# Kernel tuning notes

Measured on AMD Instinct MI355X. Metric: run time of the kernel, lower is better.

The kernel has to match this reference:

```python
import jax, jax.numpy as jnp
import numpy as np

B, C, D, H = 2, 1024, 1024, 16
DH = D // H
EPS = 1e-8


def setup_inputs() -> dict:
    key = jax.random.key(0)
    ks = jax.random.split(key, 12)
    s = 0.02
    return {
        "x": jax.random.normal(ks[0], (B, C, D), dtype=jnp.float32),
        "rms_w": jnp.ones((C, D), dtype=jnp.float32),
        "rms_b": jnp.zeros((C, D), dtype=jnp.float32),
        "Wqkv": jax.random.normal(ks[1], (3 * D, D), dtype=jnp.float32) * s,
        "Wout": jax.random.normal(ks[2], (D, D), dtype=jnp.float32) * s,
        "bout": jnp.zeros((D,), dtype=jnp.float32),
        "Wf": jax.random.normal(ks[3], (D, D), dtype=jnp.float32) * s,
        "bf": jnp.zeros((D,), dtype=jnp.float32),
        "Ww": jax.random.normal(ks[4], (D, D), dtype=jnp.float32) * s,
        "bw": jnp.zeros((D,), dtype=jnp.float32),
        "Wv": jax.random.normal(ks[5], (D, D), dtype=jnp.float32) * s,
        "bv": jnp.zeros((D,), dtype=jnp.float32),
        "beta": jnp.ones((1,), dtype=jnp.float32),
    }


def _rope_cos_sin(C, dh):
    # faithful to source: theta = 10000 ** (-2*(i-1)/dh), i in [0, dh//2)
    i = jnp.arange(dh // 2, dtype=jnp.float32)
    theta = 10000.0 ** (-2.0 * (i - 1.0) / dh)            # [dh//2]
    ang = jnp.arange(C, dtype=jnp.float32)[:, None] * theta  # [C, dh//2]
    return jnp.cos(ang), jnp.sin(ang)


def _rotate(t, cos, sin):
    # equivalent to einsum('bhci,cij->bhcj', t, R) with the source R
    ev, od = t[..., 0::2], t[..., 1::2]          # [B,H,C,dh//2]
    out_ev = ev * cos + od * sin
    out_od = -ev * sin + od * cos
    return jnp.stack([out_ev, out_od], axis=-1).reshape(t.shape)


def _rmsnorm(x, w, b):
    rms = jnp.sqrt(jnp.mean(x * x, axis=-1, keepdims=True) + EPS)
    return w * (x / rms) + b


def _attention(x, Wqkv, Wout, bout):
    qkv = x @ Wqkv.T                               # [B,C,3D]
    q, k, v = jnp.split(qkv, 3, axis=-1)
    def heads(t):
        return t.reshape(B, C, H, DH).transpose(0, 2, 1, 3)  # [B,H,C,dh]
    q, k, v = heads(q), heads(k), heads(v)
    cos, sin = _rope_cos_sin(C, DH)
    qr = _rotate(q, cos, sin)
    kr = _rotate(k, cos, sin)
    scale = 1.0 / jnp.sqrt(jnp.float32(DH))
    num = jnp.exp(jnp.einsum('bhid,bhjd->bhij', qr, kr) * scale)
    den = jnp.sum(jnp.exp(jnp.einsum('bhid,bhjd->bhij', q, k) * scale),
                  axis=-1, keepdims=True)
    attn = num / den
    mask = jnp.tril(jnp.ones((C, C), dtype=bool))
    attn = jnp.where(mask[None, None], attn, 0.0)
    y = attn @ v                                   # [B,H,C,dh]
    y = y.transpose(0, 2, 1, 3).reshape(B, C, D)
    return y @ Wout.T + bout


def _ffn(x, Wf, bf, Ww, bw, Wv, bv, beta):
    h = x @ Wf.T + bf
    wx = h @ Ww.T + bw
    swish = wx * jax.nn.sigmoid(beta * wx)
    return swish * (h @ Wv.T + bv)


def reference(x, rms_w, rms_b, Wqkv, Wout, bout, Wf, bf, Ww, bw, Wv, bv, beta):
    # dropout p is identity in eval mode
    x = _rmsnorm(x, rms_w, rms_b)
    x = x + _attention(x, Wqkv, Wout, bout)
    x = _rmsnorm(x, rms_w, rms_b)   # same shared RMSNorm module applied twice
    x = x + _ffn(x, Wf, bf, Ww, bw, Wv, bv, beta)
    return x
```

## Files before the change

### kernel.cpp

```cpp
#include <hip/hip_runtime.h>
#include <math.h>

#define B_ 2
#define C_ 1024
#define D_ 1024
#define H_ 16
#define DH_ 64
#define EPSF 1e-8f
#define BK 32

typedef __bf16 bf16;
typedef __attribute__((ext_vector_type(4))) __bf16 bf16x4;
typedef __attribute__((ext_vector_type(8))) __bf16 bf16x8;
typedef __attribute__((ext_vector_type(4))) float f32x4;

__device__ inline f32x4 mfma16(bf16x8 a, bf16x8 b, f32x4 c) {
  return __builtin_amdgcn_mfma_f32_16x16x32_bf16(a, b, c, 0, 0, 0);
}

__device__ inline void async16(const bf16* g, bf16* l) {
  __builtin_amdgcn_global_load_lds((const __attribute__((address_space(1))) void*)g,
                                   (__attribute__((address_space(3))) void*)l, 16, 0, 0);
}

__device__ inline float rope_theta(float i) {
  return exp2f(-13.287712379549449f * (2.0f * (i - 1.0f) * (1.0f / 64.0f)));
}

__global__ __launch_bounds__(256) void cvt_rms_kernel(const float* __restrict__ wqkv,
                                                      const float* __restrict__ wout,
                                                      const float* __restrict__ wf,
                                                      const float* __restrict__ www,
                                                      const float* __restrict__ wv,
                                                      bf16* __restrict__ wdst,
                                                      const float* __restrict__ x,
                                                      const float* __restrict__ rw,
                                                      const float* __restrict__ rb,
                                                      bf16* __restrict__ xout) {
  __shared__ float red[4];
  int t = threadIdx.x;
  if (blockIdx.x < 7 * 1024) {
    int seg = blockIdx.x >> 10;
    int local = (blockIdx.x & 1023) * 1024 + t * 4;
    const float* src = seg < 3 ? wqkv + (size_t)seg * (D_ * D_)
                     : seg == 3 ? wout : seg == 4 ? wf : seg == 5 ? www : wv;
    float4 v = *(const float4*)(src + local);
    bf16x4 o;
    o[0] = (bf16)v.x; o[1] = (bf16)v.y; o[2] = (bf16)v.z; o[3] = (bf16)v.w;
    *(bf16x4*)(wdst + (size_t)seg * (D_ * D_) + local) = o;
    return;
  }
  int row = blockIdx.x - 7 * 1024;
  int c = row & (C_ - 1);
  float4 xv = *(const float4*)(x + (size_t)row * D_ + t * 4);
  float ss = xv.x * xv.x + xv.y * xv.y + xv.z * xv.z + xv.w * xv.w;
#pragma unroll
  for (int m = 1; m < 64; m <<= 1) ss += __shfl_xor(ss, m, 64);
  if ((t & 63) == 0) red[t >> 6] = ss;
  __syncthreads();
  float tot = red[0] + red[1] + red[2] + red[3];
  float inv = rsqrtf(tot * (1.0f / D_) + EPSF);
  float4 wv4 = *(const float4*)(rw + (size_t)c * D_ + t * 4);
  float4 bv4 = *(const float4*)(rb + (size_t)c * D_ + t * 4);
  bf16x4 ov;
  ov[0] = (bf16)(wv4.x * (xv.x * inv) + bv4.x);
  ov[1] = (bf16)(wv4.y * (xv.y * inv) + bv4.y);
  ov[2] = (bf16)(wv4.z * (xv.z * inv) + bv4.z);
  ov[3] = (bf16)(wv4.w * (xv.w * inv) + bv4.w);
  *(bf16x4*)(xout + (size_t)row * D_ + t * 4) = ov;
}

__global__ __launch_bounds__(256) void rmsnorm_bf16_kernel(const bf16* __restrict__ x,
                                                           const float* __restrict__ w,
                                                           const float* __restrict__ b,
                                                           bf16* __restrict__ out) {
  int row = blockIdx.x;
  int c = row & (C_ - 1);
  int t = threadIdx.x;
  bf16x4 xv = *(const bf16x4*)(x + (size_t)row * D_ + t * 4);
  float f0 = (float)xv[0], f1 = (float)xv[1], f2 = (float)xv[2], f3 = (float)xv[3];
  float ss = f0 * f0 + f1 * f1 + f2 * f2 + f3 * f3;
#pragma unroll
  for (int m = 1; m < 64; m <<= 1) ss += __shfl_xor(ss, m, 64);
  __shared__ float red[4];
  if ((t & 63) == 0) red[t >> 6] = ss;
  __syncthreads();
  float tot = red[0] + red[1] + red[2] + red[3];
  float inv = rsqrtf(tot * (1.0f / D_) + EPSF);
  float4 wv = *(const float4*)(w + (size_t)c * D_ + t * 4);
  float4 bv = *(const float4*)(b + (size_t)c * D_ + t * 4);
  bf16x4 ov;
  ov[0] = (bf16)(wv.x * (f0 * inv) + bv.x);
  ov[1] = (bf16)(wv.y * (f1 * inv) + bv.y);
  ov[2] = (bf16)(wv.z * (f2 * inv) + bv.z);
  ov[3] = (bf16)(wv.w * (f3 * inv) + bv.w);
  *(bf16x4*)(out + (size_t)row * D_ + t * 4) = ov;
}

template <int BMt, int BNt>
__global__ __launch_bounds__(256) void gemm_lds(const bf16* __restrict__ A,
                                                const bf16* __restrict__ W,
                                                const float* __restrict__ bias,
                                                const bf16* __restrict__ R,
                                                bf16* __restrict__ Cout,
                                                int M, int N, int K) {
  constexpr int MT = BMt / 32;
  constexpr int NT = BNt / 32;
  __shared__ bf16 sa[BMt * BK];
  __shared__ bf16 sb[BNt * BK];
  int t = threadIdx.x, l = t & 63, w = t >> 6;
  int m0 = blockIdx.y * BMt;
  int n0 = blockIdx.x * BNt;
  int wm = (w >> 1) * (BMt / 2), wn = (w & 1) * (BNt / 2);
  int lm = l & 15, lq = l >> 4;
  f32x4 acc[MT][NT] = {};

  for (int k0 = 0; k0 < K; k0 += BK) {
    __syncthreads();
    if constexpr (BMt >= 64) {
#pragma unroll
      for (int p = 0; p < BMt / 64; ++p) {
        int lin = p * 256 + t;
        async16(A + (size_t)(m0 + (lin >> 2)) * K + k0 + (lin & 3) * 8, sa + lin * 8);
      }
    } else {
      if (t < BMt * 4)
        async16(A + (size_t)(m0 + (t >> 2)) * K + k0 + (t & 3) * 8, sa + t * 8);
    }
#pragma unroll
    for (int p = 0; p < BNt / 64; ++p) {
      int lin = p * 256 + t;
      async16(W + (size_t)(n0 + (lin >> 2)) * K + k0 + (lin & 3) * 8, sb + lin * 8);
    }
    __syncthreads();
    bf16x8 af[MT], bfr[NT];
#pragma unroll
    for (int mt = 0; mt < MT; ++mt)
      af[mt] = *(const bf16x8*)(sa + (wm + mt * 16 + lm) * BK + lq * 8);
#pragma unroll
    for (int nt = 0; nt < NT; ++nt)
      bfr[nt] = *(const bf16x8*)(sb + (wn + nt * 16 + lm) * BK + lq * 8);
#pragma unroll
    for (int mt = 0; mt < MT; ++mt)
#pragma unroll
      for (int nt = 0; nt < NT; ++nt)
        acc[mt][nt] = mfma16(af[mt], bfr[nt], acc[mt][nt]);
  }
#pragma unroll
  for (int mt = 0; mt < MT; ++mt)
#pragma unroll
    for (int nt = 0; nt < NT; ++nt) {
      int col = n0 + wn + nt * 16 + lm;
      float bb = bias ? bias[col] : 0.0f;
#pragma unroll
      for (int r = 0; r < 4; ++r) {
        int row = m0 + wm + mt * 16 + lq * 4 + r;
        float v = acc[mt][nt][r] + bb;
        if (R) v += (float)R[(size_t)row * N + col];
        Cout[(size_t)row * N + col] = (bf16)v;
      }
    }
}

__global__ __launch_bounds__(256) void gemm_qkv_kernel(const bf16* __restrict__ A,
                                                       const bf16* __restrict__ W,
                                                       bf16* __restrict__ qkv,
                                                       bf16* __restrict__ vt) {
  constexpr int BMt = 128, BNt = 64, MT = 4, NT = 2;
  const int N = 3 * D_, K = D_;
  __shared__ bf16 sa[BMt * BK];
  __shared__ bf16 sb[BNt * BK];
  __shared__ bf16 tv[64 * 136];
  int t = threadIdx.x, l = t & 63, w = t >> 6;
  int m0 = blockIdx.y * BMt;
  int n0 = blockIdx.x * BNt;
  int wm = (w >> 1) * 64, wn = (w & 1) * 32;
  int lm = l & 15, lq = l >> 4;
  f32x4 acc[MT][NT] = {};

  for (int k0 = 0; k0 < K; k0 += BK) {
    __syncthreads();
#pragma unroll
    for (int p = 0; p < 2; ++p) {
      int lin = p * 256 + t;
      async16(A + (size_t)(m0 + (lin >> 2)) * K + k0 + (lin & 3) * 8, sa + lin * 8);
    }
    async16(W + (size_t)(n0 + (t >> 2)) * K + k0 + (t & 3) * 8, sb + t * 8);
    __syncthreads();
    bf16x8 af[MT], bfr[NT];
#pragma unroll
    for (int mt = 0; mt < MT; ++mt)
      af[mt] = *(const bf16x8*)(sa + (wm + mt * 16 + lm) * BK + lq * 8);
#pragma unroll
    for (int nt = 0; nt < NT; ++nt)
      bfr[nt] = *(const bf16x8*)(sb + (wn + nt * 16 + lm) * BK + lq * 8);
#pragma unroll
    for (int mt = 0; mt < MT; ++mt)
#pragma unroll
      for (int nt = 0; nt < NT; ++nt)
        acc[mt][nt] = mfma16(af[mt], bfr[nt], acc[mt][nt]);
  }
  if (n0 < 2 * D_) {
#pragma unroll
    for (int mt = 0; mt < MT; ++mt)
#pragma unroll
      for (int nt = 0; nt < NT; ++nt) {
        int col = n0 + wn + nt * 16 + lm;
#pragma unroll
        for (int r = 0; r < 4; ++r) {
          int row = m0 + wm + mt * 16 + lq * 4 + r;
          qkv[(size_t)row * N + col] = (bf16)acc[mt][nt][r];
        }
      }
  } else {
#pragma unroll
    for (int mt = 0; mt < MT; ++mt)
#pragma unroll
      for (int nt = 0; nt < NT; ++nt) {
        int dh = wn + nt * 16 + lm;
#pragma unroll
        for (int r = 0; r < 4; ++r)
          tv[dh * 136 + wm + mt * 16 + lq * 4 + r] = (bf16)acc[mt][nt][r];
      }
    __syncthreads();
    int h = (n0 - 2 * D_) >> 6;
    int bb = m0 >> 10;
    int mloc = m0 & 1023;
    size_t vbase = (size_t)((bb * H_ + h) * DH_) * C_;
#pragma unroll
    for (int p = 0; p < 4; ++p) {
      int lin = p * 256 + t;
      int dh = lin >> 4;
      int mm = (lin & 15) * 8;
      *(int4*)(vt + vbase + (size_t)dh * C_ + mloc + mm) = *(int4*)(tv + dh * 136 + mm);
    }
  }
}

__global__ __launch_bounds__(256) void gemm_ffn_kernel(const bf16* __restrict__ A,
                                                       const bf16* __restrict__ Ww,
                                                       const bf16* __restrict__ Wv,
                                                       const float* __restrict__ bw,
                                                       const float* __restrict__ bv,
                                                       const bf16* __restrict__ x3,
                                                       const float* __restrict__ beta_p,
                                                       float* __restrict__ out) {
  __shared__ bf16 sa[64 * BK];
  __shared__ bf16 sb1[64 * BK];
  __shared__ bf16 sb2[64 * BK];
  int t = threadIdx.x, l = t & 63, w = t >> 6;
  int m0 = blockIdx.y * 64, n0 = blockIdx.x * 64;
  int wm = (w >> 1) * 32, wn = (w & 1) * 32;
  int lm = l & 15, lq = l >> 4;
  float beta = beta_p[0];
  f32x4 acc1[2][2] = {}, acc2[2][2] = {};

  for (int k0 = 0; k0 < D_; k0 += BK) {
    __syncthreads();
    async16(A + (size_t)(m0 + (t >> 2)) * D_ + k0 + (t & 3) * 8, sa + t * 8);
    async16(Ww + (size_t)(n0 + (t >> 2)) * D_ + k0 + (t & 3) * 8, sb1 + t * 8);
    async16(Wv + (size_t)(n0 + (t >> 2)) * D_ + k0 + (t & 3) * 8, sb2 + t * 8);
    __syncthreads();
    bf16x8 af[2], b1f[2], b2f[2];
#pragma unroll
    for (int mt = 0; mt < 2; ++mt)
      af[mt] = *(const bf16x8*)(sa + (wm + mt * 16 + lm) * BK + lq * 8);
#pragma unroll
    for (int nt = 0; nt < 2; ++nt) {
      b1f[nt] = *(const bf16x8*)(sb1 + (wn + nt * 16 + lm) * BK + lq * 8);
      b2f[nt] = *(const bf16x8*)(sb2 + (wn + nt * 16 + lm) * BK + lq * 8);
    }
#pragma unroll
    for (int mt = 0; mt < 2; ++mt)
#pragma unroll
      for (int nt = 0; nt < 2; ++nt) {
        acc1[mt][nt] = mfma16(af[mt], b1f[nt], acc1[mt][nt]);
        acc2[mt][nt] = mfma16(af[mt], b2f[nt], acc2[mt][nt]);
      }
  }
#pragma unroll
  for (int mt = 0; mt < 2; ++mt)
#pragma unroll
    for (int nt = 0; nt < 2; ++nt) {
      int col = n0 + wn + nt * 16 + lm;
      float bbw = bw[col], bbv = bv[col];
#pragma unroll
      for (int r = 0; r < 4; ++r) {
        int row = m0 + wm + mt * 16 + lq * 4 + r;
        float z = acc1[mt][nt][r] + bbw;
        float g = acc2[mt][nt][r] + bbv;
        float sw = z / (1.0f + __expf(-beta * z));
        out[(size_t)row * D_ + col] = (float)x3[(size_t)row * D_ + col] + sw * g;
      }
    }
}

__global__ __launch_bounds__(256) void attn_kernel(const bf16* __restrict__ qkv,
                                                   const bf16* __restrict__ vt,
                                                   float* __restrict__ yp,
                                                   float* __restrict__ dp) {
  __shared__ bf16 sk[64 * 72];
  __shared__ bf16 skr[64 * 72];
  __shared__ bf16 sv[64 * 72];
  __shared__ bf16 pl[4][16 * 72];
  int t = threadIdx.x, l = t & 63, w = t >> 6;
  int blk = blockIdx.x;
  int it = blk >> 6;
  int r6 = blk & 63;
  int b = r6 >> 5;
  int h = (r6 >> 1) & 15;
  int half = r6 & 1;
  int i_base = it * 64 + w * 16;
  int lm = l & 15, lq = l >> 4;
  const float scale = 0.125f;
  int jf = half << 9;

  size_t hq = (size_t)h * DH_;
  size_t qrow = (size_t)(b * C_ + i_base + lm) * (3 * D_) + hq;
  bf16x8 qp[2], qrf[2];
  float cq = (float)(i_base + lm);
#pragma unroll
  for (int kk = 0; kk < 2; ++kk) {
    qp[kk] = *(const bf16x8*)(qkv + qrow + kk * 32 + lq * 8);
#pragma unroll
    for (int j = 0; j < 4; ++j) {
      float ip = (float)(kk * 16 + lq * 4 + j);
      float ang = cq * rope_theta(ip);
      float sv_, cv_;
      __sincosf(ang, &sv_, &cv_);
      float qe = (float)qp[kk][2 * j], qo = (float)qp[kk][2 * j + 1];
      qrf[kk][2 * j] = (bf16)(qe * cv_ + qo * sv_);
      qrf[kk][2 * j + 1] = (bf16)(qo * cv_ - qe * sv_);
    }
  }

  float den[4] = {0.f, 0.f, 0.f, 0.f};
  f32x4 yacc[4] = {};
  int i_max = i_base + 15;
  size_t kbase = (size_t)(b * C_) * (3 * D_) + D_ + hq;
  size_t vtbase = (size_t)((b * H_ + h) * DH_) * C_;
  int sr = t >> 3;
  int sc = (t & 7) * 8;
  float th0 = rope_theta((float)((sc >> 1) + 0));
  float th1 = rope_theta((float)((sc >> 1) + 1));
  float th2 = rope_theta((float)((sc >> 1) + 2));
  float th3 = rope_theta((float)((sc >> 1) + 3));

  float cA0, sA0, cA1, sA1, cA2, sA2, cA3, sA3;
  float cB0, sB0, cB1, sB1, cB2, sB2, cB3, sB3;
  float C0, S0, C1, S1, C2, S2, C3, S3;
#define INITP(P)                       \
  {                                    \
    float a;                           \
    a = (float)(jf + sr) * th##P;      \
    __sincosf(a, &sA##P, &cA##P);      \
    a = (float)(jf + 32 + sr) * th##P; \
    __sincosf(a, &sB##P, &cB##P);      \
    a = 64.0f * th##P;                 \
    __sincosf(a, &S##P, &C##P);        \
  }
  INITP(0) INITP(1) INITP(2) INITP(3)
#undef INITP

  int4 pk0, pk1, pv0, pv1;
#define FETCH_TILE(J0)                                                          \
  pk0 = *(const int4*)(qkv + kbase + (size_t)((J0) + sr) * (3 * D_) + sc);      \
  pk1 = *(const int4*)(qkv + kbase + (size_t)((J0) + 32 + sr) * (3 * D_) + sc); \
  pv0 = *(const int4*)(vt + vtbase + (size_t)sr * C_ + (J0) + sc);              \
  pv1 = *(const int4*)(vt + vtbase + (size_t)(32 + sr) * C_ + (J0) + sc);

  FETCH_TILE(jf)

  for (int j0 = jf; j0 < jf + 512; j0 += 64) {
    __syncthreads();
    *(int4*)(sk + sr * 72 + sc) = pk0;
    *(int4*)(sk + (32 + sr) * 72 + sc) = pk1;
    *(int4*)(sv + sr * 72 + sc) = pv0;
    *(int4*)(sv + (32 + sr) * 72 + sc) = pv1;
    {
      bf16x8 k0 = *(bf16x8*)&pk0, k1 = *(bf16x8*)&pk1;
      bf16x8 r0, r1;
#define ROT2(KV, RV, CC, SS, J)                           \
  {                                                       \
    float e = (float)KV[2 * J], o = (float)KV[2 * J + 1]; \
    RV[2 * J] = (bf16)(e * CC + o * SS);                  \
    RV[2 * J + 1] = (bf16)(o * CC - e * SS);              \
  }
      ROT2(k0, r0, cA0, sA0, 0) ROT2(k0, r0, cA1, sA1, 1)
      ROT2(k0, r0, cA2, sA2, 2) ROT2(k0, r0, cA3, sA3, 3)
      ROT2(k1, r1, cB0, sB0, 0) ROT2(k1, r1, cB1, sB1, 1)
      ROT2(k1, r1, cB2, sB2, 2) ROT2(k1, r1, cB3, sB3, 3)
#undef ROT2
#define STEP(CX, SX, P)               \
  {                                   \
    float nc = CX * C##P - SX * S##P; \
    SX = SX * C##P + CX * S##P;       \
    CX = nc;                          \
  }
      STEP(cA0, sA0, 0) STEP(cA1, sA1, 1) STEP(cA2, sA2, 2) STEP(cA3, sA3, 3)
      STEP(cB0, sB0, 0) STEP(cB1, sB1, 1) STEP(cB2, sB2, 2) STEP(cB3, sB3, 3)
#undef STEP
      *(int4*)(skr + sr * 72 + sc) = *(int4*)&r0;
      *(int4*)(skr + (32 + sr) * 72 + sc) = *(int4*)&r1;
    }
    __syncthreads();
    if (j0 + 64 < jf + 512) {
      FETCH_TILE(j0 + 64)
    }
#pragma unroll
    for (int js = 0; js < 64; js += 16) {
      bf16x8 kf0 = *(const bf16x8*)(sk + (js + lm) * 72 + lq * 8);
      bf16x8 kf1 = *(const bf16x8*)(sk + (js + lm) * 72 + 32 + lq * 8);
      f32x4 s = {0.f, 0.f, 0.f, 0.f};
      s = mfma16(qp[0], kf0, s);
      s = mfma16(qp[1], kf1, s);
#pragma unroll
      for (int r = 0; r < 4; ++r) den[r] += __expf(s[r] * scale);
    }
    if (j0 <= i_max) {
#pragma unroll
      for (int js = 0; js < 64; js += 16) {
        bf16x8 kf0 = *(const bf16x8*)(skr + (js + lm) * 72 + lq * 8);
        bf16x8 kf1 = *(const bf16x8*)(skr + (js + lm) * 72 + 32 + lq * 8);
        f32x4 s = {0.f, 0.f, 0.f, 0.f};
        s = mfma16(qrf[0], kf0, s);
        s = mfma16(qrf[1], kf1, s);
#pragma unroll
        for (int r = 0; r < 4; ++r) {
          int jg = j0 + js + lm;
          int ig = i_base + lq * 4 + r;
          float p = (jg <= ig) ? __expf(s[r] * scale) : 0.0f;
          pl[w][(lq * 4 + r) * 72 + js + lm] = (bf16)p;
        }
      }
      __builtin_amdgcn_wave_barrier();
      bf16x8 pf0 = *(const bf16x8*)(pl[w] + lm * 72 + lq * 8);
      bf16x8 pf1 = *(const bf16x8*)(pl[w] + lm * 72 + 32 + lq * 8);
#pragma unroll
      for (int tt = 0; tt < 4; ++tt) {
        bf16x8 vf0 = *(const bf16x8*)(sv + (tt * 16 + lm) * 72 + lq * 8);
        bf16x8 vf1 = *(const bf16x8*)(sv + (tt * 16 + lm) * 72 + 32 + lq * 8);
        yacc[tt] = mfma16(pf0, vf0, mfma16(pf1, vf1, yacc[tt]));
      }
      __builtin_amdgcn_wave_barrier();
    }
  }
#undef FETCH_TILE
#pragma unroll
  for (int r = 0; r < 4; ++r) {
    float d = den[r];
    d += __shfl_xor(d, 1, 64);
    d += __shfl_xor(d, 2, 64);
    d += __shfl_xor(d, 4, 64);
    d += __shfl_xor(d, 8, 64);
    if (lm == 0) dp[(size_t)blk * 64 + w * 16 + lq * 4 + r] = d;
  }
  size_t yb = (size_t)blk * 4096;
#pragma unroll
  for (int tt = 0; tt < 4; ++tt)
#pragma unroll
    for (int r = 0; r < 4; ++r)
      yp[yb + (size_t)(w * 16 + lq * 4 + r) * 64 + tt * 16 + lm] = yacc[tt][r];
}

__global__ __launch_bounds__(256) void combine_kernel(const float* __restrict__ yp,
                                                      const float* __restrict__ dp,
                                                      bf16* __restrict__ y) {
  int cb = blockIdx.x;
  int it = cb >> 5;
  int b = (cb >> 4) & 1;
  int h = cb & 15;
  int t = threadIdx.x;
  int row = t >> 2;
  int cg = (t & 3) * 16;
  size_t p0 = (size_t)(cb * 2) * 4096 + (size_t)row * 64 + cg;
  size_t p1 = p0 + 4096;
  float inv = 1.0f / (dp[(size_t)(cb * 2) * 64 + row] + dp[(size_t)(cb * 2 + 1) * 64 + row]);
  bf16x8 o0, o1;
#pragma unroll
  for (int c = 0; c < 8; ++c) o0[c] = (bf16)((yp[p0 + c] + yp[p1 + c]) * inv);
#pragma unroll
  for (int c = 0; c < 8; ++c) o1[c] = (bf16)((yp[p0 + 8 + c] + yp[p1 + 8 + c]) * inv);
  size_t ob = (size_t)(b * C_ + it * 64 + row) * D_ + h * DH_ + cg;
  *(bf16x8*)(y + ob) = o0;
  *(bf16x8*)(y + ob + 8) = o1;
}

extern "C" void kernel_launch(void* const* d_in, const int* in_sizes, int n_in,
                              void* d_out, int out_size, void* d_ws, size_t ws_size,
                              hipStream_t stream) {
  const float* x = (const float*)d_in[0];
  const float* rms_w = (const float*)d_in[1];
  const float* rms_b = (const float*)d_in[2];
  const float* Wqkv = (const float*)d_in[3];
  const float* Wout = (const float*)d_in[4];
  const float* bout = (const float*)d_in[5];
  const float* Wf = (const float*)d_in[6];
  const float* bfp = (const float*)d_in[7];
  const float* Ww = (const float*)d_in[8];
  const float* bw = (const float*)d_in[9];
  const float* Wv = (const float*)d_in[10];
  const float* bv = (const float*)d_in[11];
  const float* beta = (const float*)d_in[12];
  float* out = (float*)d_out;

  bf16* ws = (bf16*)d_ws;
  const size_t DD = (size_t)D_ * D_;
  const size_t MC = (size_t)B_ * C_;
  bf16* wb = ws;
  bf16* x1 = ws + 7 * DD;
  bf16* qkv = ws + 9 * DD;
  bf16* vt = ws + 15 * DD;
  bf16* x2 = ws + 17 * DD;
  bf16* x3 = ws + 19 * DD;
  bf16* hbuf = ws + 21 * DD;
  float* yp = (float*)(ws + 24 * DD);
  float* dp = yp + (size_t)1024 * 4096;
  bf16* y = (bf16*)d_out;

  cvt_rms_kernel<<<7 * 1024 + MC, 256, 0, stream>>>(Wqkv, Wout, Wf, Ww, Wv, wb, x, rms_w,
                                                    rms_b, x1);
  gemm_qkv_kernel<<<dim3(3 * D_ / 64, MC / 128), 256, 0, stream>>>(x1, wb, qkv, vt);
  attn_kernel<<<B_ * H_ * 16 * 2, 256, 0, stream>>>(qkv, vt, yp, dp);
  combine_kernel<<<B_ * H_ * 16, 256, 0, stream>>>(yp, dp, y);
  gemm_lds<32, 64><<<dim3(D_ / 64, MC / 32), 256, 0, stream>>>(
      y, wb + 3 * DD, bout, x1, x2, MC, D_, D_);
  rmsnorm_bf16_kernel<<<MC, 256, 0, stream>>>(x2, rms_w, rms_b, x3);
  gemm_lds<32, 64><<<dim3(D_ / 64, MC / 32), 256, 0, stream>>>(
      x3, wb + 4 * DD, bfp, nullptr, hbuf, MC, D_, D_);
  gemm_ffn_kernel<<<dim3(D_ / 64, MC / 64), 256, 0, stream>>>(
      hbuf, wb + 5 * DD, wb + 6 * DD, bw, bv, x3, beta, out);
}
```

Before: 228.2 us.

## Drop split-K attention and combine kernel; use 64x64 tiles for projection GEMMs

Attention blocks now iterate over the full key range instead of two halves. Each block normalizes by the denominator and writes bf16 output directly, which removes the fp32 partial buffers and the separate combine kernel launch. The output and FFN-input GEMMs switch from 32x64 to 64x64 tiles. The tradeoff is fewer blocks and longer per-block serial loops, which reduces parallelism on a 256-CU device.

```diff
diff --git a/kernel.cpp b/kernel.cpp
--- a/kernel.cpp
+++ b/kernel.cpp
@@ -117,15 +117,10 @@
 
   for (int k0 = 0; k0 < K; k0 += BK) {
     __syncthreads();
-    if constexpr (BMt >= 64) {
-#pragma unroll
-      for (int p = 0; p < BMt / 64; ++p) {
-        int lin = p * 256 + t;
-        async16(A + (size_t)(m0 + (lin >> 2)) * K + k0 + (lin & 3) * 8, sa + lin * 8);
-      }
-    } else {
-      if (t < BMt * 4)
-        async16(A + (size_t)(m0 + (t >> 2)) * K + k0 + (t & 3) * 8, sa + t * 8);
+#pragma unroll
+    for (int p = 0; p < BMt / 64; ++p) {
+      int lin = p * 256 + t;
+      async16(A + (size_t)(m0 + (lin >> 2)) * K + k0 + (lin & 3) * 8, sa + lin * 8);
     }
 #pragma unroll
     for (int p = 0; p < BNt / 64; ++p) {
@@ -297,23 +292,20 @@
 
 __global__ __launch_bounds__(256) void attn_kernel(const bf16* __restrict__ qkv,
                                                    const bf16* __restrict__ vt,
-                                                   float* __restrict__ yp,
-                                                   float* __restrict__ dp) {
+                                                   bf16* __restrict__ y) {
   __shared__ bf16 sk[64 * 72];
   __shared__ bf16 skr[64 * 72];
   __shared__ bf16 sv[64 * 72];
   __shared__ bf16 pl[4][16 * 72];
   int t = threadIdx.x, l = t & 63, w = t >> 6;
   int blk = blockIdx.x;
-  int it = blk >> 6;
-  int r6 = blk & 63;
-  int b = r6 >> 5;
-  int h = (r6 >> 1) & 15;
-  int half = r6 & 1;
+  int it = blk >> 5;
+  int r5 = blk & 31;
+  int b = r5 >> 4;
+  int h = r5 & 15;
   int i_base = it * 64 + w * 16;
   int lm = l & 15, lq = l >> 4;
   const float scale = 0.125f;
-  int jf = half << 9;
 
   size_t hq = (size_t)h * DH_;
   size_t qrow = (size_t)(b * C_ + i_base + lm) * (3 * D_) + hq;
@@ -349,15 +341,15 @@
   float cA0, sA0, cA1, sA1, cA2, sA2, cA3, sA3;
   float cB0, sB0, cB1, sB1, cB2, sB2, cB3, sB3;
   float C0, S0, C1, S1, C2, S2, C3, S3;
-#define INITP(P)                       \
-  {                                    \
-    float a;                           \
-    a = (float)(jf + sr) * th##P;      \
-    __sincosf(a, &sA##P, &cA##P);      \
-    a = (float)(jf + 32 + sr) * th##P; \
-    __sincosf(a, &sB##P, &cB##P);      \
-    a = 64.0f * th##P;                 \
-    __sincosf(a, &S##P, &C##P);        \
+#define INITP(P)                  \
+  {                               \
+    float a;                      \
+    a = (float)(sr)*th##P;        \
+    __sincosf(a, &sA##P, &cA##P); \
+    a = (float)(32 + sr) * th##P; \
+    __sincosf(a, &sB##P, &cB##P); \
+    a = 64.0f * th##P;            \
+    __sincosf(a, &S##P, &C##P);   \
   }
   INITP(0) INITP(1) INITP(2) INITP(3)
 #undef INITP
@@ -369,9 +361,9 @@
   pv0 = *(const int4*)(vt + vtbase + (size_t)sr * C_ + (J0) + sc);              \
   pv1 = *(const int4*)(vt + vtbase + (size_t)(32 + sr) * C_ + (J0) + sc);
 
-  FETCH_TILE(jf)
-
-  for (int j0 = jf; j0 < jf + 512; j0 += 64) {
+  FETCH_TILE(0)
+
+  for (int j0 = 0; j0 < C_; j0 += 64) {
     __syncthreads();
     *(int4*)(sk + sr * 72 + sc) = pk0;
     *(int4*)(sk + (32 + sr) * 72 + sc) = pk1;
@@ -404,7 +396,7 @@
       *(int4*)(skr + (32 + sr) * 72 + sc) = *(int4*)&r1;
     }
     __syncthreads();
-    if (j0 + 64 < jf + 512) {
+    if (j0 + 64 < C_) {
       FETCH_TILE(j0 + 64)
     }
 #pragma unroll
@@ -446,6 +438,7 @@
     }
   }
 #undef FETCH_TILE
+  float inv[4];
 #pragma unroll
   for (int r = 0; r < 4; ++r) {
     float d = den[r];
@@ -453,37 +446,15 @@
     d += __shfl_xor(d, 2, 64);
     d += __shfl_xor(d, 4, 64);
     d += __shfl_xor(d, 8, 64);
-    if (lm == 0) dp[(size_t)blk * 64 + w * 16 + lq * 4 + r] = d;
-  }
-  size_t yb = (size_t)blk * 4096;
+    inv[r] = 1.0f / d;
+  }
 #pragma unroll
   for (int tt = 0; tt < 4; ++tt)
 #pragma unroll
-    for (int r = 0; r < 4; ++r)
-      yp[yb + (size_t)(w * 16 + lq * 4 + r) * 64 + tt * 16 + lm] = yacc[tt][r];
-}
-
-__global__ __launch_bounds__(256) void combine_kernel(const float* __restrict__ yp,
-                                                      const float* __restrict__ dp,
-                                                      bf16* __restrict__ y) {
-  int cb = blockIdx.x;
-  int it = cb >> 5;
-  int b = (cb >> 4) & 1;
-  int h = cb & 15;
-  int t = threadIdx.x;
-  int row = t >> 2;
-  int cg = (t & 3) * 16;
-  size_t p0 = (size_t)(cb * 2) * 4096 + (size_t)row * 64 + cg;
-  size_t p1 = p0 + 4096;
-  float inv = 1.0f / (dp[(size_t)(cb * 2) * 64 + row] + dp[(size_t)(cb * 2 + 1) * 64 + row]);
-  bf16x8 o0, o1;
-#pragma unroll
-  for (int c = 0; c < 8; ++c) o0[c] = (bf16)((yp[p0 + c] + yp[p1 + c]) * inv);
-#pragma unroll
-  for (int c = 0; c < 8; ++c) o1[c] = (bf16)((yp[p0 + 8 + c] + yp[p1 + 8 + c]) * inv);
-  size_t ob = (size_t)(b * C_ + it * 64 + row) * D_ + h * DH_ + cg;
-  *(bf16x8*)(y + ob) = o0;
-  *(bf16x8*)(y + ob + 8) = o1;
+    for (int r = 0; r < 4; ++r) {
+      int ig = i_base + lq * 4 + r;
+      y[(size_t)(b * C_ + ig) * D_ + hq + tt * 16 + lm] = (bf16)(yacc[tt][r] * inv[r]);
+    }
 }
 
 extern "C" void kernel_launch(void* const* d_in, const int* in_sizes, int n_in,
@@ -514,19 +485,16 @@
   bf16* x2 = ws + 17 * DD;
   bf16* x3 = ws + 19 * DD;
   bf16* hbuf = ws + 21 * DD;
-  float* yp = (float*)(ws + 24 * DD);
-  float* dp = yp + (size_t)1024 * 4096;
   bf16* y = (bf16*)d_out;
 
   cvt_rms_kernel<<<7 * 1024 + MC, 256, 0, stream>>>(Wqkv, Wout, Wf, Ww, Wv, wb, x, rms_w,
                                                     rms_b, x1);
   gemm_qkv_kernel<<<dim3(3 * D_ / 64, MC / 128), 256, 0, stream>>>(x1, wb, qkv, vt);
-  attn_kernel<<<B_ * H_ * 16 * 2, 256, 0, stream>>>(qkv, vt, yp, dp);
-  combine_kernel<<<B_ * H_ * 16, 256, 0, stream>>>(yp, dp, y);
-  gemm_lds<32, 64><<<dim3(D_ / 64, MC / 32), 256, 0, stream>>>(
+  attn_kernel<<<B_ * H_ * 16, 256, 0, stream>>>(qkv, vt, y);
+  gemm_lds<64, 64><<<dim3(D_ / 64, MC / 64), 256, 0, stream>>>(
       y, wb + 3 * DD, bout, x1, x2, MC, D_, D_);
   rmsnorm_bf16_kernel<<<MC, 256, 0, stream>>>(x2, rms_w, rms_b, x3);
-  gemm_lds<32, 64><<<dim3(D_ / 64, MC / 32), 256, 0, stream>>>(
+  gemm_lds<64, 64><<<dim3(D_ / 64, MC / 64), 256, 0, stream>>>(
       x3, wb + 4 * DD, bfp, nullptr, hbuf, MC, D_, D_);
   gemm_ffn_kernel<<<dim3(D_ / 64, MC / 64), 256, 0, stream>>>(
       hbuf, wb + 5 * DD, wb + 6 * DD, bw, bv, x3, beta, out);
```

After: 221.6 us. -2.9%, faster.
